# Kernel optimization log

Hardware: AMD Instinct MI355X
Metric: run time of the kernel (lower is better)

The kernel has to match this reference:

```python
import jax, jax.numpy as jnp
import numpy as np

DIM = 768
HEADS = 12
HEAD_DIM = DIM // HEADS
SCALE = HEAD_DIM ** -0.5


def setup_inputs() -> dict:
    key = jax.random.key(0)
    ks = jax.random.split(key, 5)
    x = jax.random.normal(ks[0], (2, 4096, DIM), dtype=jnp.float32)
    # torch nn.Linear params: weight [out, in], bias [out]
    qkv_w = jax.random.normal(ks[1], (3 * DIM, DIM), dtype=jnp.float32) * (DIM ** -0.5)
    qkv_b = jax.random.normal(ks[2], (3 * DIM,), dtype=jnp.float32) * 0.02
    proj_w = jax.random.normal(ks[3], (DIM, DIM), dtype=jnp.float32) * (DIM ** -0.5)
    proj_b = jax.random.normal(ks[4], (DIM,), dtype=jnp.float32) * 0.02
    return {"x": x, "qkv_w": qkv_w, "qkv_b": qkv_b, "proj_w": proj_w, "proj_b": proj_b}


def reference(x, qkv_w, qkv_b, proj_w, proj_b):
    b, n, c = x.shape
    qkv = x @ qkv_w.T + qkv_b                      # [b, n, 3c]
    qkv = qkv.reshape(b, n, 3, HEADS, HEAD_DIM)
    qkv = jnp.transpose(qkv, (2, 0, 3, 1, 4))      # [3, b, h, n, d]
    q, k, v = qkv[0], qkv[1], qkv[2]
    attn = jax.nn.softmax(jnp.einsum('bhqd,bhkd->bhqk', q, k) * SCALE, axis=-1)
    out = jnp.einsum('bhqk,bhkd->bhqd', attn, v)   # [b, h, n, d]
    out = jnp.transpose(out, (0, 2, 1, 3)).reshape(b, n, c)
    return out @ proj_w.T + proj_b
```

## Files before the change

kernel.cpp:

```cpp
#include <hip/hip_runtime.h>
#include <stdint.h>

#define SEQ   4096
#define NDIM  768
#define HD    64
#define NH    12
#define NBH   24
#define MTOT  8192

#define PSTR 72

typedef short s8v __attribute__((ext_vector_type(8)));
typedef float f4v __attribute__((ext_vector_type(4)));
typedef float f16x __attribute__((ext_vector_type(16)));
typedef unsigned short u16;
typedef u16 u16x4 __attribute__((ext_vector_type(4)));
typedef uint32_t u32x4v __attribute__((ext_vector_type(4)));
typedef int i32x2 __attribute__((ext_vector_type(2)));

#define C1 0.18033688011112042f

__device__ __forceinline__ u16 f2bf(float f) {
  union { float f; uint32_t u; } cv; cv.f = f;
  const uint32_t u = cv.u;
  return (u16)((u + 0x7fffu + ((u >> 16) & 1u)) >> 16);
}
__device__ __forceinline__ float ex2(float x) { return __builtin_amdgcn_exp2f(x); }

__device__ __forceinline__ uint32_t cvtpk_bf16(float lo, float hi) {
  uint32_t r;
  asm("v_cvt_pk_bf16_f32 %0, %1, %2" : "=v"(r) : "v"(lo), "v"(hi));
  return r;
}
__device__ __forceinline__ void pl32swap(uint32_t& a, uint32_t& b) {
  i32x2 r = __builtin_amdgcn_permlane32_swap((int)a, (int)b, false, false);
  a = (uint32_t)r.x; b = (uint32_t)r.y;
}
__device__ __forceinline__ void gload_lds16(const void* g, void* l) {
  __builtin_amdgcn_global_load_lds(
      (const __attribute__((address_space(1))) uint32_t*)g,
      (__attribute__((address_space(3))) uint32_t*)l, 16, 0, 0);
}

__global__ __launch_bounds__(256) void cvt3_kernel(
    const float* __restrict__ a, u16* __restrict__ da, int na4,
    const float* __restrict__ b, u16* __restrict__ db, int nb4,
    const float* __restrict__ c, u16* __restrict__ dc, int nc4) {
  int i = blockIdx.x * 256 + threadIdx.x;
  const float* s; u16* d;
  if (i < na4)             { s = a; d = da; }
  else if (i < na4 + nb4)  { s = b; d = db; i -= na4; }
  else if (i < na4 + nb4 + nc4) { s = c; d = dc; i -= na4 + nb4; }
  else return;
  const float4 f = ((const float4*)s)[i];
  u16x4 r;
  r[0] = f2bf(f.x); r[1] = f2bf(f.y); r[2] = f2bf(f.z); r[3] = f2bf(f.w);
  ((u16x4*)d)[i] = r;
}

__global__ __launch_bounds__(256) void gemm_qkv(const u16* __restrict__ A,
    const u16* __restrict__ B, const float* __restrict__ bias,
    u16* __restrict__ qtg, u16* __restrict__ kg, u16* __restrict__ vtg) {
  __shared__ __align__(16) u16 at[128 * 64];
  __shared__ __align__(16) u16 bt[128 * 64];
  const int tid  = threadIdx.x;
  const int lane = tid & 63;
  const int w    = tid >> 6;
  const int quad = lane >> 4;
  const int col  = lane & 15;
  const int bid  = blockIdx.x;
  const int wgid = (bid & 7) * 144 + (bid >> 3);
  const int n0 = (wgid % 18) * 128;
  const int m0 = (wgid / 18) * 128;
  const int lrow = lane >> 3;
  const int lchk = ((lane & 7) ^ lrow) * 8;
  const int wm = (w >> 1) * 64;
  const int wn = (w & 1) * 64;
  const int c7 = col & 7;

  const f4v fz = {0.f, 0.f, 0.f, 0.f};
  f4v acc[4][4];
#pragma unroll
  for (int i = 0; i < 4; i++)
#pragma unroll
    for (int j = 0; j < 4; j++) acc[i][j] = fz;

  const u16* ga = A + (size_t)(m0 + w * 32 + lrow) * NDIM + lchk;
  const u16* gb = B + (size_t)(n0 + w * 32 + lrow) * NDIM + lchk;
  u16* const la = at + (size_t)w * 2048;
  u16* const lb = bt + (size_t)w * 2048;

  for (int k0 = 0; k0 < NDIM; k0 += 64) {
    __syncthreads();
    gload_lds16(ga + k0, la);
    gload_lds16(ga + (size_t)8 * NDIM + k0, la + 512);
    gload_lds16(ga + (size_t)16 * NDIM + k0, la + 1024);
    gload_lds16(ga + (size_t)24 * NDIM + k0, la + 1536);
    gload_lds16(gb + k0, lb);
    gload_lds16(gb + (size_t)8 * NDIM + k0, lb + 512);
    gload_lds16(gb + (size_t)16 * NDIM + k0, lb + 1024);
    gload_lds16(gb + (size_t)24 * NDIM + k0, lb + 1536);
    __syncthreads();
#pragma unroll
    for (int kk = 0; kk < 2; kk++) {
      const int xo = ((kk * 4 + quad) ^ c7) * 8;
      s8v af[4], bf[4];
#pragma unroll
      for (int i = 0; i < 4; i++)
        af[i] = *(const s8v*)(at + (wm + i * 16 + col) * 64 + xo);
#pragma unroll
      for (int j = 0; j < 4; j++)
        bf[j] = *(const s8v*)(bt + (wn + j * 16 + col) * 64 + xo);
#pragma unroll
      for (int i = 0; i < 4; i++)
#pragma unroll
        for (int j = 0; j < 4; j++)
          acc[i][j] = __builtin_amdgcn_mfma_f32_16x16x32_bf16(af[i], bf[j], acc[i][j], 0, 0, 0);
    }
  }

  const int wmg = m0 + wm;
  const int wng = n0 + wn;
  const int s = n0 / NDIM;
#pragma unroll
  for (int j = 0; j < 4; j++) {
    const int c = wng + j * 16 + col;
    const float bv = bias[c];
    const int r = c - s * NDIM;
    const int h = r >> 6;
    const int d = r & 63;
#pragma unroll
    for (int i = 0; i < 4; i++) {
      const int mb = wmg + i * 16 + quad * 4;
      const int bb = mb >> 12;
      const int n  = mb & 4095;
      const size_t hb = (size_t)(bb * NH + h);
      const f4v v = acc[i][j];
      if (s == 2) {
        u16x4 pk;
#pragma unroll
        for (int rg = 0; rg < 4; rg++) pk[rg] = f2bf(v[rg] + bv);
        *(u16x4*)(vtg + (hb * HD + d) * SEQ + n) = pk;
      } else if (s == 0) {
        u16x4 pk;
#pragma unroll
        for (int rg = 0; rg < 4; rg++) pk[rg] = f2bf((v[rg] + bv) * C1);
        *(u16x4*)(qtg + (hb * HD + d) * SEQ + n) = pk;
      } else {
#pragma unroll
        for (int rg = 0; rg < 4; rg++)
          kg[(hb * SEQ + (size_t)(n + rg)) * HD + d] = f2bf(v[rg] + bv);
      }
    }
  }
}

__global__ __launch_bounds__(256, 3) void attn_kernel(const u16* __restrict__ qtg,
    const u16* __restrict__ kg, const u16* __restrict__ vtg, u16* __restrict__ og) {
  __shared__ __align__(16) u16 kls[2][64 * PSTR];
  __shared__ __align__(16) u16 vls[2][64 * PSTR];
  __shared__ float lws[4][32];

  const int tid  = threadIdx.x;
  const int lane = tid & 63;
  const int w    = tid >> 6;
  const int hi   = lane >> 5;
  const int c    = lane & 31;
  const int blk = blockIdx.x;
  const int bh  = blk % NBH;
  const int q0  = (blk / NBH) * 128;
  const size_t gbase = (size_t)bh * (SEQ * HD);
  const int wq = w * 32;

  s8v qf[4];
  {
    const u16* qp = qtg + gbase + (q0 + wq + c);
#pragma unroll
    for (int s = 0; s < 4; s++) {
      s8v t;
#pragma unroll
      for (int j = 0; j < 8; j++)
        t[j] = (short)qp[(size_t)(s * 16 + hi * 8 + j) * SEQ];
      qf[s] = t;
    }
  }

  f16x zacc;
#pragma unroll
  for (int e = 0; e < 16; e++) zacc[e] = 0.f;
  f16x o0 = zacc, o1 = zacc;
  float l0 = 0.f, l1 = 0.f, l2 = 0.f, l3 = 0.f;

  const int srow8 = tid >> 3;
  const int sch8  = (tid & 7) * 8;
  const u16* kp = kg  + gbase + (size_t)srow8 * HD  + sch8;
  const u16* vp = vtg + gbase + (size_t)srow8 * SEQ;

  s8v kr0 = *(const s8v*)(kp);
  s8v kr1 = *(const s8v*)(kp + (size_t)32 * HD);
  s8v vr0 = *(const s8v*)(vp + sch8);
  s8v vr1 = *(const s8v*)(vp + (size_t)32 * SEQ + sch8);
  *(s8v*)(kls[0] + srow8 * PSTR + sch8) = kr0;
  *(s8v*)(kls[0] + (32 + srow8) * PSTR + sch8) = kr1;
  *(s8v*)(vls[0] + srow8 * PSTR + sch8) = vr0;
  *(s8v*)(vls[0] + (32 + srow8) * PSTR + sch8) = vr1;

  for (int kb = 0; kb < SEQ; kb += 64) {
    const int cur = (kb >> 6) & 1;
    const u16* kt_ = kls[cur];
    const u16* vt_ = vls[cur];
    __syncthreads();

    if (kb + 64 < SEQ) {
      kr0 = *(const s8v*)(kp + (size_t)(kb + 64) * HD);
      kr1 = *(const s8v*)(kp + (size_t)(kb + 96) * HD);
      vr0 = *(const s8v*)(vp + kb + 64 + sch8);
      vr1 = *(const s8v*)(vp + (size_t)32 * SEQ + kb + 64 + sch8);
    }

    __builtin_amdgcn_s_setprio(1);
    f16x st0, st1;
    {
      const s8v k0_ = *(const s8v*)(kt_ + c * PSTR + hi * 8);
      const s8v k1_ = *(const s8v*)(kt_ + (32 + c) * PSTR + hi * 8);
      st0 = __builtin_amdgcn_mfma_f32_32x32x16_bf16(k0_, qf[0], zacc, 0, 0, 0);
      st1 = __builtin_amdgcn_mfma_f32_32x32x16_bf16(k1_, qf[0], zacc, 0, 0, 0);
    }
#pragma unroll
    for (int s = 1; s < 4; s++) {
      const s8v k0_ = *(const s8v*)(kt_ + c * PSTR + s * 16 + hi * 8);
      const s8v k1_ = *(const s8v*)(kt_ + (32 + c) * PSTR + s * 16 + hi * 8);
      st0 = __builtin_amdgcn_mfma_f32_32x32x16_bf16(k0_, qf[s], st0, 0, 0, 0);
      st1 = __builtin_amdgcn_mfma_f32_32x32x16_bf16(k1_, qf[s], st1, 0, 0, 0);
    }
    __builtin_amdgcn_s_setprio(0);

    s8v pa0, pa1, pa2, pa3;
    {
      float p[16];
#pragma unroll
      for (int e = 0; e < 16; e++) p[e] = ex2(st0[e]);
      l0 += p[0] + p[4] + p[8]  + p[12];
      l1 += p[1] + p[5] + p[9]  + p[13];
      l2 += p[2] + p[6] + p[10] + p[14];
      l3 += p[3] + p[7] + p[11] + p[15];
      uint32_t k0 = cvtpk_bf16(p[0],  p[1]);
      uint32_t k1 = cvtpk_bf16(p[2],  p[3]);
      uint32_t k2 = cvtpk_bf16(p[4],  p[5]);
      uint32_t k3 = cvtpk_bf16(p[6],  p[7]);
      uint32_t k4 = cvtpk_bf16(p[8],  p[9]);
      uint32_t k5 = cvtpk_bf16(p[10], p[11]);
      uint32_t k6 = cvtpk_bf16(p[12], p[13]);
      uint32_t k7 = cvtpk_bf16(p[14], p[15]);
      pl32swap(k0, k2); pl32swap(k1, k3);
      pl32swap(k4, k6); pl32swap(k5, k7);
      u32x4v wA = {k0, k1, k2, k3};
      u32x4v wB = {k4, k5, k6, k7};
      pa0 = __builtin_bit_cast(s8v, wA);
      pa1 = __builtin_bit_cast(s8v, wB);
    }

    __builtin_amdgcn_s_setprio(1);
    {
      const s8v v00 = *(const s8v*)(vt_ + c * PSTR + hi * 8);
      const s8v v01 = *(const s8v*)(vt_ + (32 + c) * PSTR + hi * 8);
      const s8v v10 = *(const s8v*)(vt_ + c * PSTR + 16 + hi * 8);
      const s8v v11 = *(const s8v*)(vt_ + (32 + c) * PSTR + 16 + hi * 8);
      o0 = __builtin_amdgcn_mfma_f32_32x32x16_bf16(pa0, v00, o0, 0, 0, 0);
      o1 = __builtin_amdgcn_mfma_f32_32x32x16_bf16(pa0, v01, o1, 0, 0, 0);
      o0 = __builtin_amdgcn_mfma_f32_32x32x16_bf16(pa1, v10, o0, 0, 0, 0);
      o1 = __builtin_amdgcn_mfma_f32_32x32x16_bf16(pa1, v11, o1, 0, 0, 0);
    }
    __builtin_amdgcn_s_setprio(0);

    {
      float p[16];
#pragma unroll
      for (int e = 0; e < 16; e++) p[e] = ex2(st1[e]);
      l0 += p[0] + p[4] + p[8]  + p[12];
      l1 += p[1] + p[5] + p[9]  + p[13];
      l2 += p[2] + p[6] + p[10] + p[14];
      l3 += p[3] + p[7] + p[11] + p[15];
      uint32_t k0 = cvtpk_bf16(p[0],  p[1]);
      uint32_t k1 = cvtpk_bf16(p[2],  p[3]);
      uint32_t k2 = cvtpk_bf16(p[4],  p[5]);
      uint32_t k3 = cvtpk_bf16(p[6],  p[7]);
      uint32_t k4 = cvtpk_bf16(p[8],  p[9]);
      uint32_t k5 = cvtpk_bf16(p[10], p[11]);
      uint32_t k6 = cvtpk_bf16(p[12], p[13]);
      uint32_t k7 = cvtpk_bf16(p[14], p[15]);
      pl32swap(k0, k2); pl32swap(k1, k3);
      pl32swap(k4, k6); pl32swap(k5, k7);
      u32x4v wA = {k0, k1, k2, k3};
      u32x4v wB = {k4, k5, k6, k7};
      pa2 = __builtin_bit_cast(s8v, wA);
      pa3 = __builtin_bit_cast(s8v, wB);
    }

    if (kb + 64 < SEQ) {
      u16* kn = (u16*)kls[cur ^ 1];
      u16* vn = (u16*)vls[cur ^ 1];
      *(s8v*)(kn + srow8 * PSTR + sch8) = kr0;
      *(s8v*)(kn + (32 + srow8) * PSTR + sch8) = kr1;
      *(s8v*)(vn + srow8 * PSTR + sch8) = vr0;
      *(s8v*)(vn + (32 + srow8) * PSTR + sch8) = vr1;
    }

    __builtin_amdgcn_s_setprio(1);
    {
      const s8v v20 = *(const s8v*)(vt_ + c * PSTR + 32 + hi * 8);
      const s8v v21 = *(const s8v*)(vt_ + (32 + c) * PSTR + 32 + hi * 8);
      const s8v v30 = *(const s8v*)(vt_ + c * PSTR + 48 + hi * 8);
      const s8v v31 = *(const s8v*)(vt_ + (32 + c) * PSTR + 48 + hi * 8);
      o0 = __builtin_amdgcn_mfma_f32_32x32x16_bf16(pa2, v20, o0, 0, 0, 0);
      o1 = __builtin_amdgcn_mfma_f32_32x32x16_bf16(pa2, v21, o1, 0, 0, 0);
      o0 = __builtin_amdgcn_mfma_f32_32x32x16_bf16(pa3, v30, o0, 0, 0, 0);
      o1 = __builtin_amdgcn_mfma_f32_32x32x16_bf16(pa3, v31, o1, 0, 0, 0);
    }
    __builtin_amdgcn_s_setprio(0);
  }

  float lt = l0 + l1 + l2 + l3;
  lt += __shfl_xor(lt, 32);
  const float inv = 1.0f / lt;
  if (hi == 0) lws[w][c] = inv;

  const int b = bh / NH;
  const int h = bh % NH;
  u16* obase = og + (size_t)(b * SEQ + q0 + wq) * NDIM + h * HD + c;
#pragma unroll
  for (int r = 0; r < 16; r++) {
    const int row = (r & 3) + 8 * (r >> 2) + 4 * hi;
    const float invr = lws[w][row];
    u16* rp = obase + (size_t)row * NDIM;
    rp[0]  = f2bf(o0[r] * invr);
    rp[32] = f2bf(o1[r] * invr);
  }
}

__global__ __launch_bounds__(256) void gemm_proj(const u16* __restrict__ A,
    const u16* __restrict__ B, const float* __restrict__ bias, float* __restrict__ out) {
  __shared__ __align__(16) u16 at[128 * 64];
  __shared__ __align__(16) u16 bt[128 * 64];
  const int tid  = threadIdx.x;
  const int lane = tid & 63;
  const int w    = tid >> 6;
  const int quad = lane >> 4;
  const int col  = lane & 15;
  const int bid  = blockIdx.x;
  const int wgid = (bid & 7) * 48 + (bid >> 3);
  const int n0 = (wgid % 6) * 128;
  const int m0 = (wgid / 6) * 128;
  const int lrow = lane >> 3;
  const int lchk = ((lane & 7) ^ lrow) * 8;
  const int wm = (w >> 1) * 64;
  const int wn = (w & 1) * 64;
  const int c7 = col & 7;

  const f4v fz = {0.f, 0.f, 0.f, 0.f};
  f4v acc[4][4];
#pragma unroll
  for (int i = 0; i < 4; i++)
#pragma unroll
    for (int j = 0; j < 4; j++) acc[i][j] = fz;

  const u16* ga = A + (size_t)(m0 + w * 32 + lrow) * NDIM + lchk;
  const u16* gb = B + (size_t)(n0 + w * 32 + lrow) * NDIM + lchk;
  u16* const la = at + (size_t)w * 2048;
  u16* const lb = bt + (size_t)w * 2048;

  for (int k0 = 0; k0 < NDIM; k0 += 64) {
    __syncthreads();
    gload_lds16(ga + k0, la);
    gload_lds16(ga + (size_t)8 * NDIM + k0, la + 512);
    gload_lds16(ga + (size_t)16 * NDIM + k0, la + 1024);
    gload_lds16(ga + (size_t)24 * NDIM + k0, la + 1536);
    gload_lds16(gb + k0, lb);
    gload_lds16(gb + (size_t)8 * NDIM + k0, lb + 512);
    gload_lds16(gb + (size_t)16 * NDIM + k0, lb + 1024);
    gload_lds16(gb + (size_t)24 * NDIM + k0, lb + 1536);
    __syncthreads();
#pragma unroll
    for (int kk = 0; kk < 2; kk++) {
      const int xo = ((kk * 4 + quad) ^ c7) * 8;
      s8v af[4], bf[4];
#pragma unroll
      for (int i = 0; i < 4; i++)
        af[i] = *(const s8v*)(at + (wm + i * 16 + col) * 64 + xo);
#pragma unroll
      for (int j = 0; j < 4; j++)
        bf[j] = *(const s8v*)(bt + (wn + j * 16 + col) * 64 + xo);
#pragma unroll
      for (int i = 0; i < 4; i++)
#pragma unroll
        for (int j = 0; j < 4; j++)
          acc[i][j] = __builtin_amdgcn_mfma_f32_16x16x32_bf16(af[i], bf[j], acc[i][j], 0, 0, 0);
    }
  }

  const int wmg = m0 + wm;
  const int wng = n0 + wn;
#pragma unroll
  for (int j = 0; j < 4; j++) {
    const int c = wng + j * 16 + col;
    const float bv = bias[c];
#pragma unroll
    for (int i = 0; i < 4; i++) {
#pragma unroll
      for (int rg = 0; rg < 4; rg++)
        out[(size_t)(wmg + i * 16 + quad * 4 + rg) * NDIM + c] = acc[i][j][rg] + bv;
    }
  }
}

extern "C" void kernel_launch(void* const* d_in, const int* in_sizes, int n_in,
                              void* d_out, int out_size, void* d_ws, size_t ws_size,
                              hipStream_t stream) {
  const float* x      = (const float*)d_in[0];
  const float* qkv_w  = (const float*)d_in[1];
  const float* qkv_b  = (const float*)d_in[2];
  const float* proj_w = (const float*)d_in[3];
  const float* proj_b = (const float*)d_in[4];
  float* out = (float*)d_out;

  u16* ws   = (u16*)d_ws;
  u16* x_bf = ws;
  u16* wq   = x_bf + (size_t)MTOT * NDIM;
  u16* wp   = wq + (size_t)3 * NDIM * NDIM;
  u16* qt   = wp + (size_t)NDIM * NDIM;
  u16* k_bf = qt + (size_t)NBH * SEQ * HD;
  u16* vt   = k_bf + (size_t)NBH * SEQ * HD;
  u16* a_bf = vt + (size_t)NBH * SEQ * HD;

  const int nx = MTOT * NDIM / 4, nw1 = 3 * NDIM * NDIM / 4, nw2 = NDIM * NDIM / 4;
  const int ntot = nx + nw1 + nw2;
  cvt3_kernel<<<(ntot + 255) / 256, 256, 0, stream>>>(x, x_bf, nx, qkv_w, wq, nw1,
                                                      proj_w, wp, nw2);

  gemm_qkv<<<1152, 256, 0, stream>>>(x_bf, wq, qkv_b, qt, k_bf, vt);
  attn_kernel<<<768, 256, 0, stream>>>(qt, k_bf, vt, a_bf);
  gemm_proj<<<384, 256, 0, stream>>>(a_bf, wp, proj_b, out);
}
```

Measured before the change: 261.1 us.

## Double-buffer GEMM LDS tiles with register-staged prefetch in QKV and proj kernels

Both GEMM kernels drop direct global-to-LDS loads and use register-staged loads into double-buffered, padded LDS tiles (K step 32, stride 40) with one barrier per iteration. The next tile's global loads are issued before the current MFMAs, and its LDS stores sit between the two halves of the MFMA work, with s_setprio raising wave priority around the matrix ops. The aim is to hide global load latency and halve the barriers per K step, at the cost of more K iterations, extra VGPRs for the staged data, and padding in place of the XOR swizzle.

Result: slower. 270.2 us (+3.5%).

```diff
diff --git a/kernel.cpp b/kernel.cpp
--- a/kernel.cpp
+++ b/kernel.cpp
@@ -8,6 +8,7 @@
 #define NBH   24
 #define MTOT  8192
 
+#define LSTR 40
 #define PSTR 72
 
 typedef short s8v __attribute__((ext_vector_type(8)));
@@ -35,11 +36,6 @@
 __device__ __forceinline__ void pl32swap(uint32_t& a, uint32_t& b) {
   i32x2 r = __builtin_amdgcn_permlane32_swap((int)a, (int)b, false, false);
   a = (uint32_t)r.x; b = (uint32_t)r.y;
-}
-__device__ __forceinline__ void gload_lds16(const void* g, void* l) {
-  __builtin_amdgcn_global_load_lds(
-      (const __attribute__((address_space(1))) uint32_t*)g,
-      (__attribute__((address_space(3))) uint32_t*)l, 16, 0, 0);
 }
 
 __global__ __launch_bounds__(256) void cvt3_kernel(
@@ -61,8 +57,8 @@
 __global__ __launch_bounds__(256) void gemm_qkv(const u16* __restrict__ A,
     const u16* __restrict__ B, const float* __restrict__ bias,
     u16* __restrict__ qtg, u16* __restrict__ kg, u16* __restrict__ vtg) {
-  __shared__ __align__(16) u16 at[128 * 64];
-  __shared__ __align__(16) u16 bt[128 * 64];
+  __shared__ __align__(16) u16 at[2][128 * LSTR];
+  __shared__ __align__(16) u16 bt[2][128 * LSTR];
   const int tid  = threadIdx.x;
   const int lane = tid & 63;
   const int w    = tid >> 6;
@@ -72,11 +68,10 @@
   const int wgid = (bid & 7) * 144 + (bid >> 3);
   const int n0 = (wgid % 18) * 128;
   const int m0 = (wgid / 18) * 128;
-  const int lrow = lane >> 3;
-  const int lchk = ((lane & 7) ^ lrow) * 8;
+  const int srow = tid >> 2;
+  const int sch  = (tid & 3) * 8;
   const int wm = (w >> 1) * 64;
   const int wn = (w & 1) * 64;
-  const int c7 = col & 7;
 
   const f4v fz = {0.f, 0.f, 0.f, 0.f};
   f4v acc[4][4];
@@ -85,38 +80,65 @@
 #pragma unroll
     for (int j = 0; j < 4; j++) acc[i][j] = fz;
 
-  const u16* ga = A + (size_t)(m0 + w * 32 + lrow) * NDIM + lchk;
-  const u16* gb = B + (size_t)(n0 + w * 32 + lrow) * NDIM + lchk;
-  u16* const la = at + (size_t)w * 2048;
-  u16* const lb = bt + (size_t)w * 2048;
-
-  for (int k0 = 0; k0 < NDIM; k0 += 64) {
+  const u16* ap0 = A + (size_t)(m0 + srow) * NDIM + sch;
+  const u16* ap1 = A + (size_t)(m0 + 64 + srow) * NDIM + sch;
+  const u16* bp0 = B + (size_t)(n0 + srow) * NDIM + sch;
+  const u16* bp1 = B + (size_t)(n0 + 64 + srow) * NDIM + sch;
+
+  s8v ar0 = *(const s8v*)(ap0);
+  s8v ar1 = *(const s8v*)(ap1);
+  s8v br0 = *(const s8v*)(bp0);
+  s8v br1 = *(const s8v*)(bp1);
+  *(s8v*)(at[0] + srow * LSTR + sch) = ar0;
+  *(s8v*)(at[0] + (64 + srow) * LSTR + sch) = ar1;
+  *(s8v*)(bt[0] + srow * LSTR + sch) = br0;
+  *(s8v*)(bt[0] + (64 + srow) * LSTR + sch) = br1;
+
+  for (int k0 = 0; k0 < NDIM; k0 += 32) {
+    const int cur = (k0 >> 5) & 1;
+    const u16* at_ = at[cur];
+    const u16* bt_ = bt[cur];
     __syncthreads();
-    gload_lds16(ga + k0, la);
-    gload_lds16(ga + (size_t)8 * NDIM + k0, la + 512);
-    gload_lds16(ga + (size_t)16 * NDIM + k0, la + 1024);
-    gload_lds16(ga + (size_t)24 * NDIM + k0, la + 1536);
-    gload_lds16(gb + k0, lb);
-    gload_lds16(gb + (size_t)8 * NDIM + k0, lb + 512);
-    gload_lds16(gb + (size_t)16 * NDIM + k0, lb + 1024);
-    gload_lds16(gb + (size_t)24 * NDIM + k0, lb + 1536);
-    __syncthreads();
-#pragma unroll
-    for (int kk = 0; kk < 2; kk++) {
-      const int xo = ((kk * 4 + quad) ^ c7) * 8;
-      s8v af[4], bf[4];
-#pragma unroll
-      for (int i = 0; i < 4; i++)
-        af[i] = *(const s8v*)(at + (wm + i * 16 + col) * 64 + xo);
+
+    if (k0 + 32 < NDIM) {
+      ar0 = *(const s8v*)(ap0 + k0 + 32);
+      ar1 = *(const s8v*)(ap1 + k0 + 32);
+      br0 = *(const s8v*)(bp0 + k0 + 32);
+      br1 = *(const s8v*)(bp1 + k0 + 32);
+    }
+
+    s8v af[4], bf[4];
+#pragma unroll
+    for (int i = 0; i < 4; i++)
+      af[i] = *(const s8v*)(at_ + (wm + i * 16 + col) * LSTR + quad * 8);
+#pragma unroll
+    for (int j = 0; j < 4; j++)
+      bf[j] = *(const s8v*)(bt_ + (wn + j * 16 + col) * LSTR + quad * 8);
+
+    __builtin_amdgcn_s_setprio(1);
+#pragma unroll
+    for (int i = 0; i < 2; i++)
 #pragma unroll
       for (int j = 0; j < 4; j++)
-        bf[j] = *(const s8v*)(bt + (wn + j * 16 + col) * 64 + xo);
-#pragma unroll
-      for (int i = 0; i < 4; i++)
-#pragma unroll
-        for (int j = 0; j < 4; j++)
-          acc[i][j] = __builtin_amdgcn_mfma_f32_16x16x32_bf16(af[i], bf[j], acc[i][j], 0, 0, 0);
-    }
+        acc[i][j] = __builtin_amdgcn_mfma_f32_16x16x32_bf16(af[i], bf[j], acc[i][j], 0, 0, 0);
+    __builtin_amdgcn_s_setprio(0);
+
+    if (k0 + 32 < NDIM) {
+      u16* an = (u16*)at[cur ^ 1];
+      u16* bn = (u16*)bt[cur ^ 1];
+      *(s8v*)(an + srow * LSTR + sch) = ar0;
+      *(s8v*)(an + (64 + srow) * LSTR + sch) = ar1;
+      *(s8v*)(bn + srow * LSTR + sch) = br0;
+      *(s8v*)(bn + (64 + srow) * LSTR + sch) = br1;
+    }
+
+    __builtin_amdgcn_s_setprio(1);
+#pragma unroll
+    for (int i = 2; i < 4; i++)
+#pragma unroll
+      for (int j = 0; j < 4; j++)
+        acc[i][j] = __builtin_amdgcn_mfma_f32_16x16x32_bf16(af[i], bf[j], acc[i][j], 0, 0, 0);
+    __builtin_amdgcn_s_setprio(0);
   }
 
   const int wmg = m0 + wm;
@@ -340,8 +362,8 @@
 
 __global__ __launch_bounds__(256) void gemm_proj(const u16* __restrict__ A,
     const u16* __restrict__ B, const float* __restrict__ bias, float* __restrict__ out) {
-  __shared__ __align__(16) u16 at[128 * 64];
-  __shared__ __align__(16) u16 bt[128 * 64];
+  __shared__ __align__(16) u16 at[2][128 * LSTR];
+  __shared__ __align__(16) u16 bt[2][128 * LSTR];
   const int tid  = threadIdx.x;
   const int lane = tid & 63;
   const int w    = tid >> 6;
@@ -351,11 +373,10 @@
   const int wgid = (bid & 7) * 48 + (bid >> 3);
   const int n0 = (wgid % 6) * 128;
   const int m0 = (wgid / 6) * 128;
-  const int lrow = lane >> 3;
-  const int lchk = ((lane & 7) ^ lrow) * 8;
+  const int srow = tid >> 2;
+  const int sch  = (tid & 3) * 8;
   const int wm = (w >> 1) * 64;
   const int wn = (w & 1) * 64;
-  const int c7 = col & 7;
 
   const f4v fz = {0.f, 0.f, 0.f, 0.f};
   f4v acc[4][4];
@@ -364,38 +385,65 @@
 #pragma unroll
     for (int j = 0; j < 4; j++) acc[i][j] = fz;
 
-  const u16* ga = A + (size_t)(m0 + w * 32 + lrow) * NDIM + lchk;
-  const u16* gb = B + (size_t)(n0 + w * 32 + lrow) * NDIM + lchk;
-  u16* const la = at + (size_t)w * 2048;
-  u16* const lb = bt + (size_t)w * 2048;
-
-  for (int k0 = 0; k0 < NDIM; k0 += 64) {
+  const u16* ap0 = A + (size_t)(m0 + srow) * NDIM + sch;
+  const u16* ap1 = A + (size_t)(m0 + 64 + srow) * NDIM + sch;
+  const u16* bp0 = B + (size_t)(n0 + srow) * NDIM + sch;
+  const u16* bp1 = B + (size_t)(n0 + 64 + srow) * NDIM + sch;
+
+  s8v ar0 = *(const s8v*)(ap0);
+  s8v ar1 = *(const s8v*)(ap1);
+  s8v br0 = *(const s8v*)(bp0);
+  s8v br1 = *(const s8v*)(bp1);
+  *(s8v*)(at[0] + srow * LSTR + sch) = ar0;
+  *(s8v*)(at[0] + (64 + srow) * LSTR + sch) = ar1;
+  *(s8v*)(bt[0] + srow * LSTR + sch) = br0;
+  *(s8v*)(bt[0] + (64 + srow) * LSTR + sch) = br1;
+
+  for (int k0 = 0; k0 < NDIM; k0 += 32) {
+    const int cur = (k0 >> 5) & 1;
+    const u16* at_ = at[cur];
+    const u16* bt_ = bt[cur];
     __syncthreads();
-    gload_lds16(ga + k0, la);
-    gload_lds16(ga + (size_t)8 * NDIM + k0, la + 512);
-    gload_lds16(ga + (size_t)16 * NDIM + k0, la + 1024);
-    gload_lds16(ga + (size_t)24 * NDIM + k0, la + 1536);
-    gload_lds16(gb + k0, lb);
-    gload_lds16(gb + (size_t)8 * NDIM + k0, lb + 512);
-    gload_lds16(gb + (size_t)16 * NDIM + k0, lb + 1024);
-    gload_lds16(gb + (size_t)24 * NDIM + k0, lb + 1536);
-    __syncthreads();
-#pragma unroll
-    for (int kk = 0; kk < 2; kk++) {
-      const int xo = ((kk * 4 + quad) ^ c7) * 8;
-      s8v af[4], bf[4];
-#pragma unroll
-      for (int i = 0; i < 4; i++)
-        af[i] = *(const s8v*)(at + (wm + i * 16 + col) * 64 + xo);
+
+    if (k0 + 32 < NDIM) {
+      ar0 = *(const s8v*)(ap0 + k0 + 32);
+      ar1 = *(const s8v*)(ap1 + k0 + 32);
+      br0 = *(const s8v*)(bp0 + k0 + 32);
+      br1 = *(const s8v*)(bp1 + k0 + 32);
+    }
+
+    s8v af[4], bf[4];
+#pragma unroll
+    for (int i = 0; i < 4; i++)
+      af[i] = *(const s8v*)(at_ + (wm + i * 16 + col) * LSTR + quad * 8);
+#pragma unroll
+    for (int j = 0; j < 4; j++)
+      bf[j] = *(const s8v*)(bt_ + (wn + j * 16 + col) * LSTR + quad * 8);
+
+    __builtin_amdgcn_s_setprio(1);
+#pragma unroll
+    for (int i = 0; i < 2; i++)
 #pragma unroll
       for (int j = 0; j < 4; j++)
-        bf[j] = *(const s8v*)(bt + (wn + j * 16 + col) * 64 + xo);
-#pragma unroll
-      for (int i = 0; i < 4; i++)
-#pragma unroll
-        for (int j = 0; j < 4; j++)
-          acc[i][j] = __builtin_amdgcn_mfma_f32_16x16x32_bf16(af[i], bf[j], acc[i][j], 0, 0, 0);
-    }
+        acc[i][j] = __builtin_amdgcn_mfma_f32_16x16x32_bf16(af[i], bf[j], acc[i][j], 0, 0, 0);
+    __builtin_amdgcn_s_setprio(0);
+
+    if (k0 + 32 < NDIM) {
+      u16* an = (u16*)at[cur ^ 1];
+      u16* bn = (u16*)bt[cur ^ 1];
+      *(s8v*)(an + srow * LSTR + sch) = ar0;
+      *(s8v*)(an + (64 + srow) * LSTR + sch) = ar1;
+      *(s8v*)(bn + srow * LSTR + sch) = br0;
+      *(s8v*)(bn + (64 + srow) * LSTR + sch) = br1;
+    }
+
+    __builtin_amdgcn_s_setprio(1);
+#pragma unroll
+    for (int i = 2; i < 4; i++)
+#pragma unroll
+      for (int j = 0; j < 4; j++)
+        acc[i][j] = __builtin_amdgcn_mfma_f32_16x16x32_bf16(af[i], bf[j], acc[i][j], 0, 0, 0);
+    __builtin_amdgcn_s_setprio(0);
   }
 
   const int wmg = m0 + wm;
```
